# Performance work log

Measured on AMD Instinct MI355X. Metric: run time of the kernel, lower is better.

## Reference

```python
import jax, jax.numpy as jnp
import numpy as np

SEQ, B, IN, H, GATES = 2048, 64, 64, 128, 4 * 128


def setup_inputs() -> dict:
    key = jax.random.key(0)
    ks = jax.random.split(key, 12)
    s_in = 1.0 / np.sqrt(H)
    return {
        "data": jax.random.normal(ks[0], (SEQ, B, IN), dtype=jnp.float32),
        "Wih0": jax.random.normal(ks[1], (GATES, IN), dtype=jnp.float32) * s_in,
        "Whh0": jax.random.normal(ks[2], (GATES, H), dtype=jnp.float32) * s_in,
        "bih0": jax.random.normal(ks[3], (GATES,), dtype=jnp.float32) * s_in,
        "bhh0": jax.random.normal(ks[4], (GATES,), dtype=jnp.float32) * s_in,
        "Wih1": jax.random.normal(ks[5], (GATES, H), dtype=jnp.float32) * s_in,
        "Whh1": jax.random.normal(ks[6], (GATES, H), dtype=jnp.float32) * s_in,
        "bih1": jax.random.normal(ks[7], (GATES,), dtype=jnp.float32) * s_in,
        "bhh1": jax.random.normal(ks[8], (GATES,), dtype=jnp.float32) * s_in,
        "Wlin": jax.random.normal(ks[9], (1, H), dtype=jnp.float32) * s_in,
        "blin": jax.random.normal(ks[10], (1,), dtype=jnp.float32) * s_in,
    }


def _lstm_layer(x, Wih, Whh, bih, bhh):
    # x: [T, B, D_in]; torch gate order: i, f, g, o
    Bsz = x.shape[1]
    Hd = Whh.shape[1]
    b = bih + bhh
    # Precompute input projections for all timesteps in one big GEMM: [T, B, 4H]
    xproj = jnp.einsum('tbd,gd->tbg', x, Wih) + b

    def step(carry, xp_t):
        h, c = carry
        gates = xp_t + h @ Whh.T  # [B, 4H]
        i, f, g, o = jnp.split(gates, 4, axis=-1)
        i = jax.nn.sigmoid(i)
        f = jax.nn.sigmoid(f)
        g = jnp.tanh(g)
        o = jax.nn.sigmoid(o)
        c = f * c + i * g
        h = o * jnp.tanh(c)
        return (h, c), h

    h0 = jnp.zeros((Bsz, Hd), x.dtype)
    (_, _), ys = jax.lax.scan(step, (h0, h0), xproj)
    return ys  # [T, B, H]


def reference(data, Wih0, Whh0, bih0, bhh0, Wih1, Whh1, bih1, bhh1, Wlin, blin):
    h = _lstm_layer(data, Wih0, Whh0, bih0, bhh0)
    h = _lstm_layer(h, Wih1, Whh1, bih1, bhh1)
    vecs = h @ Wlin.T + blin  # [T, B, 1]
    # NOTE: original module computes tanh(vecs) but returns the pre-tanh vecs.
    return vecs
```

## Files before the change

### kernel.cpp

```cpp
#include <hip/hip_runtime.h>

#define SEQ_T 2048
#define BATCH 64

typedef _Float16 half2v __attribute__((ext_vector_type(2)));
typedef float floatx2 __attribute__((ext_vector_type(2)));

#if defined(__has_builtin)
#  if __has_builtin(__builtin_amdgcn_fdot2)
#    define HAVE_FDOT2 1
#  endif
#endif

__device__ __forceinline__ float fdot2f(half2v a, half2v b, float c) {
#ifdef HAVE_FDOT2
  return __builtin_amdgcn_fdot2(a, b, c, false);
#else
  return c + (float)a[0] * (float)b[0] + (float)a[1] * (float)b[1];
#endif
}

__device__ __forceinline__ floatx2 fma2(floatx2 a, floatx2 b, floatx2 c) {
#if __has_builtin(__builtin_elementwise_fma)
  return __builtin_elementwise_fma(a, b, c);
#else
  floatx2 r;
  r.x = __builtin_fmaf(a.x, b.x, c.x);
  r.y = __builtin_fmaf(a.y, b.y, c.y);
  return r;
#endif
}

__device__ __forceinline__ unsigned int h2u(half2v v) { return __builtin_bit_cast(unsigned int, v); }
__device__ __forceinline__ half2v u2h(unsigned int u) { return __builtin_bit_cast(half2v, u); }

template <int K, bool IN_F32>
__global__ __launch_bounds__(512) void xproj_gemm(
    const void* __restrict__ Xv,
    const float* __restrict__ W,
    const float* __restrict__ bih, const float* __restrict__ bhh,
    unsigned short* __restrict__ xp)
{
  constexpr int MT = 64;
  const int g = threadIdx.x;
  const size_t m0 = (size_t)blockIdx.x * MT;

  __shared__ __align__(16) _Float16 xs[MT * K];

  if constexpr (IN_F32) {
    constexpr int PER = MT * K / 512;
    const float* Xf = (const float*)Xv + m0 * K + (size_t)g * PER;
    _Float16* dst = xs + g * PER;
#pragma unroll
    for (int i = 0; i < PER; i += 4) {
      float4 v = *reinterpret_cast<const float4*>(Xf + i);
      half2v h01; h01[0] = (_Float16)v.x; h01[1] = (_Float16)v.y;
      half2v h23; h23[0] = (_Float16)v.z; h23[1] = (_Float16)v.w;
      uint2 u; u.x = h2u(h01); u.y = h2u(h23);
      *reinterpret_cast<uint2*>(dst + i) = u;
    }
  } else {
    constexpr int PER = MT * K / 512;
    const unsigned short* Xh = (const unsigned short*)Xv + m0 * K + (size_t)g * PER;
#pragma unroll
    for (int i = 0; i < PER / 8; i++)
      reinterpret_cast<uint4*>(xs + g * PER)[i] = reinterpret_cast<const uint4*>(Xh)[i];
  }

  half2v wr[K / 2];
  {
    const float2* p = reinterpret_cast<const float2*>(W + (size_t)g * K);
#pragma unroll
    for (int k = 0; k < K / 2; k++) {
      float2 f = p[k];
      half2v v; v[0] = (_Float16)f.x; v[1] = (_Float16)f.y;
      wr[k] = v;
    }
  }
  const float bias = bih[g] + bhh[g];
  const int out_off = (g & 127) * 4 + (g >> 7);
  __syncthreads();

#pragma unroll 1
  for (int tb = 0; tb < MT; tb++) {
    const uint4* xv = reinterpret_cast<const uint4*>(xs + tb * K);
    float a0 = bias, a1 = 0.f, a2 = 0.f, a3 = 0.f;
#pragma unroll
    for (int i = 0; i < K / 8; i++) {
      const uint4 u = xv[i];
      a0 = fdot2f(wr[4 * i + 0], u2h(u.x), a0);
      a1 = fdot2f(wr[4 * i + 1], u2h(u.y), a1);
      a2 = fdot2f(wr[4 * i + 2], u2h(u.z), a2);
      a3 = fdot2f(wr[4 * i + 3], u2h(u.w), a3);
    }
    const float s = (a0 + a1) + (a2 + a3);
    xp[(m0 + tb) * 512 + out_off] = __builtin_bit_cast(unsigned short, (_Float16)s);
  }
}

struct StepCtx {
  int ks, r, hidx;
  int li0, li1, li2, li3;
  float sc, am, ab;
  bool writer;
};

__device__ __forceinline__ float sigmoid_fast(float x) {
  return 1.f / (1.f + __expf(-x));
}

__device__ __forceinline__ void lstm_step(
    int cur, const StepCtx& cx,
    const floatx2 (&wh)[4][16], float (&hbuf)[2][144],
    unsigned short& pf, const unsigned short*& pf_ptr,
    float& c, unsigned short*& hout_ptr)
{
  const float xpv = (float)__builtin_bit_cast(_Float16, pf);
  pf = *pf_ptr;
  pf_ptr += 2 * BATCH * 512;

  floatx2 a0 = {0.f, 0.f}, a1 = {0.f, 0.f}, a2 = {0.f, 0.f}, a3 = {0.f, 0.f};
  const float4* hv = reinterpret_cast<const float4*>(&hbuf[cur][cx.ks * 36]);
#pragma unroll
  for (int i = 0; i < 8; i++) {
    const float4 u = hv[i];
    floatx2 lo; lo.x = u.x; lo.y = u.y;
    floatx2 hi; hi.x = u.z; hi.y = u.w;
    a0 = fma2(wh[0][2 * i], lo, a0); a0 = fma2(wh[0][2 * i + 1], hi, a0);
    a1 = fma2(wh[1][2 * i], lo, a1); a1 = fma2(wh[1][2 * i + 1], hi, a1);
    a2 = fma2(wh[2][2 * i], lo, a2); a2 = fma2(wh[2][2 * i + 1], hi, a2);
    a3 = fma2(wh[3][2 * i], lo, a3); a3 = fma2(wh[3][2 * i + 1], hi, a3);
  }
  float b0v = a0.x + a0.y;
  float b1v = a1.x + a1.y;
  float b2v = a2.x + a2.y;
  float b3v = a3.x + a3.y;

  const bool q0 = (cx.ks & 1) != 0, q1 = (cx.ks & 2) != 0;
  float s0 = q0 ? b0v : b1v;
  float s1 = q0 ? b2v : b3v;
  float r0 = __shfl_xor(s0, 1);
  float r1 = __shfl_xor(s1, 1);
  float kA = (q0 ? b1v : b0v) + r0;
  float kB = (q0 ? b3v : b2v) + r1;
  float s2 = q1 ? kA : kB;
  float r2 = __shfl_xor(s2, 2);
  float sum = (q1 ? kB : kA) + r2 + xpv;

  float y = cx.am * sigmoid_fast(cx.sc * sum) + cx.ab;

  float gi = __shfl(y, cx.li0);
  float gf = __shfl(y, cx.li1);
  float gg = __shfl(y, cx.li2);
  float go = __shfl(y, cx.li3);

  c = gf * c + gi * gg;
  float th = 2.f * sigmoid_fast(2.f * c) - 1.f;
  float h = go * th;

  if (cx.writer) {
    hbuf[cur ^ 1][cx.hidx] = h;
    *hout_ptr = __builtin_bit_cast(unsigned short, (_Float16)h);
  }
  hout_ptr += BATCH * 128;

  __syncthreads();
}

__global__ __launch_bounds__(512)
__attribute__((amdgpu_waves_per_eu(2, 2)))
void lstm_rec2(
    const float* __restrict__ Whh,
    const unsigned short* __restrict__ xp,
    unsigned short* __restrict__ hout)
{
  const int b = blockIdx.x;
  const int tid = threadIdx.x;
  const int l = tid & 63;
  const int w = tid >> 6;
  const int rr = l >> 2;
  const int ks = l & 3;
  const int r = w * 16 + rr;

  __shared__ __align__(16) float hbuf[2][144];

  floatx2 wh[4][16];
#pragma unroll
  for (int g = 0; g < 4; g++) {
    const float4* p = reinterpret_cast<const float4*>(
        Whh + ((size_t)(g * 128 + r)) * 128 + ks * 32);
#pragma unroll
    for (int k = 0; k < 8; k++) {
      float4 f = p[k];
      floatx2 lo; lo.x = f.x; lo.y = f.y;
      floatx2 hi; hi.x = f.z; hi.y = f.w;
      wh[g][2 * k] = lo;
      wh[g][2 * k + 1] = hi;
    }
  }

  StepCtx cx;
  cx.ks = ks; cx.r = r;
  cx.hidx = (r >> 5) * 36 + (r & 31);
  const int lb = l & ~3;
  cx.li0 = lb + 0; cx.li1 = lb + 1; cx.li2 = lb + 2; cx.li3 = lb + 3;
  cx.sc = (ks == 2) ? 2.f : 1.f;
  cx.am = (ks == 2) ? 2.f : 1.f;
  cx.ab = (ks == 2) ? -1.f : 0.f;
  cx.writer = (ks == 0);

  if (tid < 144) { hbuf[0][tid] = 0.f; }

  const unsigned short* xpb = xp + (size_t)b * 512 + tid;
  unsigned short pfa = xpb[0];
  unsigned short pfb = xpb[(size_t)1 * (BATCH * 512)];
  const unsigned short* pA = xpb + (size_t)2 * (BATCH * 512);
  const unsigned short* pB = xpb + (size_t)3 * (BATCH * 512);
  unsigned short* houtp = hout + (size_t)b * 128 + r;
  float c = 0.f;
  __syncthreads();

#pragma unroll 1
  for (int t = 0; t < SEQ_T; t += 2) {
    lstm_step(0, cx, wh, hbuf, pfa, pA, c, houtp);
    lstm_step(1, cx, wh, hbuf, pfb, pB, c, houtp);
  }
}

__global__ __launch_bounds__(256) void final_lin(
    const unsigned short* __restrict__ h1,
    const float* __restrict__ Wlin, const float* __restrict__ blin,
    float* __restrict__ out)
{
  const size_t tb = (size_t)blockIdx.x * 256 + threadIdx.x;
  half2v wl[64];
  const float2* p = reinterpret_cast<const float2*>(Wlin);
#pragma unroll
  for (int k = 0; k < 64; k++) {
    float2 f = p[k];
    half2v v; v[0] = (_Float16)f.x; v[1] = (_Float16)f.y;
    wl[k] = v;
  }
  const uint4* hv = reinterpret_cast<const uint4*>(h1 + tb * 128);
  float a0 = 0.f, a1 = 0.f, a2 = 0.f, a3 = 0.f;
#pragma unroll
  for (int i = 0; i < 16; i++) {
    const uint4 u = hv[i];
    a0 = fdot2f(wl[4 * i + 0], u2h(u.x), a0);
    a1 = fdot2f(wl[4 * i + 1], u2h(u.y), a1);
    a2 = fdot2f(wl[4 * i + 2], u2h(u.z), a2);
    a3 = fdot2f(wl[4 * i + 3], u2h(u.w), a3);
  }
  out[tb] = (a0 + a1) + (a2 + a3) + blin[0];
}

extern "C" void kernel_launch(void* const* d_in, const int* in_sizes, int n_in,
                              void* d_out, int out_size, void* d_ws, size_t ws_size,
                              hipStream_t stream) {
  (void)in_sizes; (void)n_in; (void)out_size; (void)ws_size;

  const float* data = (const float*)d_in[0];
  const float* Wih0 = (const float*)d_in[1];
  const float* Whh0 = (const float*)d_in[2];
  const float* bih0 = (const float*)d_in[3];
  const float* bhh0 = (const float*)d_in[4];
  const float* Wih1 = (const float*)d_in[5];
  const float* Whh1 = (const float*)d_in[6];
  const float* bih1 = (const float*)d_in[7];
  const float* bhh1 = (const float*)d_in[8];
  const float* Wlin = (const float*)d_in[9];
  const float* blin = (const float*)d_in[10];

  unsigned char* ws = (unsigned char*)d_ws;
  unsigned short* xpb = (unsigned short*)ws;
  unsigned short* h0 = (unsigned short*)(ws + (size_t)128 * 1024 * 1024);
  unsigned short* h1 = (unsigned short*)(ws + (size_t)160 * 1024 * 1024);

  const int M = SEQ_T * BATCH;
  const int gemm_blocks = M / 64;

  xproj_gemm<64, true><<<dim3(gemm_blocks), dim3(512), 0, stream>>>(
      data, Wih0, bih0, bhh0, xpb);
  lstm_rec2<<<dim3(BATCH), dim3(512), 0, stream>>>(Whh0, xpb, h0);
  xproj_gemm<128, false><<<dim3(gemm_blocks), dim3(512), 0, stream>>>(
      h0, Wih1, bih1, bhh1, xpb);
  lstm_rec2<<<dim3(BATCH), dim3(512), 0, stream>>>(Whh1, xpb, h1);
  final_lin<<<dim3(M / 256), dim3(256), 0, stream>>>(h1, Wlin, blin, (float*)d_out);
}
```

Before: 3.202 ms.

## Store recurrent weights as fp16 in registers and use DPP quad permutes

```diff
diff --git a/kernel.cpp b/kernel.cpp
--- a/kernel.cpp
+++ b/kernel.cpp
@@ -20,19 +20,21 @@
 #endif
 }
 
-__device__ __forceinline__ floatx2 fma2(floatx2 a, floatx2 b, floatx2 c) {
-#if __has_builtin(__builtin_elementwise_fma)
-  return __builtin_elementwise_fma(a, b, c);
-#else
-  floatx2 r;
-  r.x = __builtin_fmaf(a.x, b.x, c.x);
-  r.y = __builtin_fmaf(a.y, b.y, c.y);
-  return r;
-#endif
-}
-
 __device__ __forceinline__ unsigned int h2u(half2v v) { return __builtin_bit_cast(unsigned int, v); }
 __device__ __forceinline__ half2v u2h(unsigned int u) { return __builtin_bit_cast(half2v, u); }
+
+template <int CTRL>
+__device__ __forceinline__ float qperm(float x) {
+  int xi = __builtin_bit_cast(int, x);
+  int ri = __builtin_amdgcn_update_dpp(xi, xi, CTRL, 0xF, 0xF, true);
+  return __builtin_bit_cast(float, ri);
+}
+#define QP_XOR1 0xB1
+#define QP_XOR2 0x4E
+#define QP_B0   0x00
+#define QP_B1   0x55
+#define QP_B2   0xAA
+#define QP_B3   0xFF
 
 template <int K, bool IN_F32>
 __global__ __launch_bounds__(512) void xproj_gemm(
@@ -100,7 +102,6 @@
 
 struct StepCtx {
   int ks, r, hidx;
-  int li0, li1, li2, li3;
   float sc, am, ab;
   bool writer;
 };
@@ -111,7 +112,7 @@
 
 __device__ __forceinline__ void lstm_step(
     int cur, const StepCtx& cx,
-    const floatx2 (&wh)[4][16], float (&hbuf)[2][144],
+    const half2v (&wh)[4][16], float (&hbuf)[2][144],
     unsigned short& pf, const unsigned short*& pf_ptr,
     float& c, unsigned short*& hout_ptr)
 {
@@ -119,40 +120,50 @@
   pf = *pf_ptr;
   pf_ptr += 2 * BATCH * 512;
 
-  floatx2 a0 = {0.f, 0.f}, a1 = {0.f, 0.f}, a2 = {0.f, 0.f}, a3 = {0.f, 0.f};
+  float a0 = 0.f, a1 = 0.f, a2 = 0.f, a3 = 0.f;
   const float4* hv = reinterpret_cast<const float4*>(&hbuf[cur][cx.ks * 36]);
 #pragma unroll
   for (int i = 0; i < 8; i++) {
     const float4 u = hv[i];
-    floatx2 lo; lo.x = u.x; lo.y = u.y;
-    floatx2 hi; hi.x = u.z; hi.y = u.w;
-    a0 = fma2(wh[0][2 * i], lo, a0); a0 = fma2(wh[0][2 * i + 1], hi, a0);
-    a1 = fma2(wh[1][2 * i], lo, a1); a1 = fma2(wh[1][2 * i + 1], hi, a1);
-    a2 = fma2(wh[2][2 * i], lo, a2); a2 = fma2(wh[2][2 * i + 1], hi, a2);
-    a3 = fma2(wh[3][2 * i], lo, a3); a3 = fma2(wh[3][2 * i + 1], hi, a3);
-  }
-  float b0v = a0.x + a0.y;
-  float b1v = a1.x + a1.y;
-  float b2v = a2.x + a2.y;
-  float b3v = a3.x + a3.y;
+    {
+      const half2v wa = wh[0][2 * i], wb = wh[0][2 * i + 1];
+      a0 = fmaf((float)wa[0], u.x, a0); a0 = fmaf((float)wa[1], u.y, a0);
+      a0 = fmaf((float)wb[0], u.z, a0); a0 = fmaf((float)wb[1], u.w, a0);
+    }
+    {
+      const half2v wa = wh[1][2 * i], wb = wh[1][2 * i + 1];
+      a1 = fmaf((float)wa[0], u.x, a1); a1 = fmaf((float)wa[1], u.y, a1);
+      a1 = fmaf((float)wb[0], u.z, a1); a1 = fmaf((float)wb[1], u.w, a1);
+    }
+    {
+      const half2v wa = wh[2][2 * i], wb = wh[2][2 * i + 1];
+      a2 = fmaf((float)wa[0], u.x, a2); a2 = fmaf((float)wa[1], u.y, a2);
+      a2 = fmaf((float)wb[0], u.z, a2); a2 = fmaf((float)wb[1], u.w, a2);
+    }
+    {
+      const half2v wa = wh[3][2 * i], wb = wh[3][2 * i + 1];
+      a3 = fmaf((float)wa[0], u.x, a3); a3 = fmaf((float)wa[1], u.y, a3);
+      a3 = fmaf((float)wb[0], u.z, a3); a3 = fmaf((float)wb[1], u.w, a3);
+    }
+  }
 
   const bool q0 = (cx.ks & 1) != 0, q1 = (cx.ks & 2) != 0;
-  float s0 = q0 ? b0v : b1v;
-  float s1 = q0 ? b2v : b3v;
-  float r0 = __shfl_xor(s0, 1);
-  float r1 = __shfl_xor(s1, 1);
-  float kA = (q0 ? b1v : b0v) + r0;
-  float kB = (q0 ? b3v : b2v) + r1;
+  float s0 = q0 ? a0 : a1;
+  float s1 = q0 ? a2 : a3;
+  float r0 = qperm<QP_XOR1>(s0);
+  float r1 = qperm<QP_XOR1>(s1);
+  float kA = (q0 ? a1 : a0) + r0;
+  float kB = (q0 ? a3 : a2) + r1;
   float s2 = q1 ? kA : kB;
-  float r2 = __shfl_xor(s2, 2);
+  float r2 = qperm<QP_XOR2>(s2);
   float sum = (q1 ? kB : kA) + r2 + xpv;
 
   float y = cx.am * sigmoid_fast(cx.sc * sum) + cx.ab;
 
-  float gi = __shfl(y, cx.li0);
-  float gf = __shfl(y, cx.li1);
-  float gg = __shfl(y, cx.li2);
-  float go = __shfl(y, cx.li3);
+  float gi = qperm<QP_B0>(y);
+  float gf = qperm<QP_B1>(y);
+  float gg = qperm<QP_B2>(y);
+  float go = qperm<QP_B3>(y);
 
   c = gf * c + gi * gg;
   float th = 2.f * sigmoid_fast(2.f * c) - 1.f;
@@ -184,7 +195,7 @@
 
   __shared__ __align__(16) float hbuf[2][144];
 
-  floatx2 wh[4][16];
+  half2v wh[4][16];
 #pragma unroll
   for (int g = 0; g < 4; g++) {
     const float4* p = reinterpret_cast<const float4*>(
@@ -192,8 +203,8 @@
 #pragma unroll
     for (int k = 0; k < 8; k++) {
       float4 f = p[k];
-      floatx2 lo; lo.x = f.x; lo.y = f.y;
-      floatx2 hi; hi.x = f.z; hi.y = f.w;
+      half2v lo; lo[0] = (_Float16)f.x; lo[1] = (_Float16)f.y;
+      half2v hi; hi[0] = (_Float16)f.z; hi[1] = (_Float16)f.w;
       wh[g][2 * k] = lo;
       wh[g][2 * k + 1] = hi;
     }
@@ -202,8 +213,6 @@
   StepCtx cx;
   cx.ks = ks; cx.r = r;
   cx.hidx = (r >> 5) * 36 + (r & 31);
-  const int lb = l & ~3;
-  cx.li0 = lb + 0; cx.li1 = lb + 1; cx.li2 = lb + 2; cx.li3 = lb + 3;
   cx.sc = (ks == 2) ? 2.f : 1.f;
   cx.am = (ks == 2) ? 2.f : 1.f;
   cx.ab = (ks == 2) ? -1.f : 0.f;
```

After: 2.752 ms. 14.0% less time.
